# Optimization experiments

Measured on AMD Instinct MI355X. Metric: run time of the kernel, lower is better.

Reference implementation:

```python
import jax, jax.numpy as jnp
import numpy as np

SCALE = 15.0
BIG = 1e9  # masked-out distances; exp(-SCALE*BIG) underflows to exactly 0 in fp32
P, M, N, D, NCAM = 6, 512, 4096, 1024, 8
FEAT_STD = 0.03  # keep squared distances O(1) so exp(-scale*d) doesn't underflow


def setup_inputs() -> dict:
    key = jax.random.key(0)
    k1, k2, k3, k4 = jax.random.split(key, 4)
    feature = jax.random.normal(k1, (P, M, D), dtype=jnp.float32) * FEAT_STD
    centers = jax.random.normal(k2, (P, N, D), dtype=jnp.float32) * FEAT_STD
    camid = jax.random.randint(k3, (M,), 0, NCAM)   # camera id per sample
    cam = jax.random.randint(k4, (N,), 0, NCAM)     # camera id per center
    return {"feature": feature, "camid": camid, "centers": centers, "cam": cam}


def _explog(x):
    # faithful to torch: (-scale * x).exp().sum().log(), per row (last axis)
    return jnp.log(jnp.sum(jnp.exp(-SCALE * x), axis=-1))


def reference(feature, camid, centers, cam):
    p, m, d = feature.shape
    n = centers.shape[1]
    # squared euclidean distance map per part: [P, m, n]
    f2 = jnp.sum(feature * feature, axis=-1)            # [P, m]
    c2 = jnp.sum(centers * centers, axis=-1)            # [P, n]
    dist = f2[:, :, None] + c2[:, None, :] - 2.0 * jnp.einsum('pmd,pnd->pmn', feature, centers)
    # intra mask: center cam == sample cam  (same for all parts)
    mask = camid[:, None] == cam[None, :]               # [m, n]
    # push masked-out entries to BIG so ascending sort puts them last and exp(-s*BIG)=0
    d_intra = jnp.sort(jnp.where(mask[None, :, :], dist, BIG), axis=-1)   # [P, m, n]
    d_inter = jnp.sort(jnp.where(mask[None, :, :], BIG, dist), axis=-1)   # [P, m, n]
    x_intra = _explog(d_intra[..., :4])
    y_intra = _explog(d_intra[..., 6:])
    x_inter = _explog(d_inter[..., :8])
    y_inter = _explog(d_inter[..., 12:])
    hinge_intra = jnp.maximum(-x_intra + y_intra + 12.0, 0.0)
    hinge_inter = jnp.maximum(-x_inter + y_inter + 5.0, 0.0)
    loss = jnp.sum(hinge_intra + hinge_inter) / (m * p)
    return loss
```

## Files before the change

### kernel.cpp

```cpp
#include <hip/hip_runtime.h>
#include <math.h>

#define PP 6
#define MM 512
#define NN 4096
#define DD 1024
#define KSCALE 15.0f
#define BIGV 1e9f

#define BM 128
#define BN 128
#define BK 32
#define NCHUNK (DD / BK)
#define NSTRIP (NN / BN)
#define KI 6
#define KR 12
#define PARTW 20

typedef __bf16 bf16x8 __attribute__((ext_vector_type(8)));
typedef float  f32x16 __attribute__((ext_vector_type(16)));

__device__ __forceinline__ void insert6(float (&a)[KI], float v) {
    if (v < a[KI - 1]) {
        float cur = v;
#pragma unroll
        for (int x = 0; x < KI; ++x) {
            float lo = fminf(a[x], cur);
            float hi = fmaxf(a[x], cur);
            a[x] = lo; cur = hi;
        }
    }
}
__device__ __forceinline__ void insert12(float (&a)[KR], float v) {
    if (v < a[KR - 1]) {
        float cur = v;
#pragma unroll
        for (int x = 0; x < KR; ++x) {
            float lo = fminf(a[x], cur);
            float hi = fmaxf(a[x], cur);
            a[x] = lo; cur = hi;
        }
    }
}

__device__ __forceinline__ void cvt8(const float4& v0, const float4& v1,
                                     bf16x8& hi, bf16x8& lo) {
    float f[8] = {v0.x, v0.y, v0.z, v0.w, v1.x, v1.y, v1.z, v1.w};
#pragma unroll
    for (int i = 0; i < 8; ++i) {
        __bf16 h = (__bf16)f[i];
        hi[i] = h;
        lo[i] = (__bf16)(f[i] - (float)h);
    }
}

__device__ __forceinline__ float sq8(const float4& a, const float4& b) {
    float s = a.x * a.x;
    s = fmaf(a.y, a.y, s); s = fmaf(a.z, a.z, s); s = fmaf(a.w, a.w, s);
    s = fmaf(b.x, b.x, s); s = fmaf(b.y, b.y, s);
    s = fmaf(b.z, b.z, s); s = fmaf(b.w, b.w, s);
    return s;
}

__global__ __launch_bounds__(256, 2)
void dist_topk_kernel(const float* __restrict__ feature,
                      const int*   __restrict__ camid,
                      const float* __restrict__ centers,
                      const int*   __restrict__ cam,
                      float*       __restrict__ partials,
                      float*       __restrict__ out) {
    const int ns = blockIdx.x;
    const int mt = blockIdx.y;
    const int p  = blockIdx.z;
    const int t  = threadIdx.x;
    const int lane = t & 63, wid = t >> 6;
    const int wr = wid >> 1, wc = wid & 1;
    const int l31 = lane & 31, lh = lane >> 5;

    __shared__ __align__(16) char smem[128 * 129 * 4];
    __shared__ float c2buf[128][4];
    __shared__ int   s_cam[128];

    if (blockIdx.x == 0 && blockIdx.y == 0 && blockIdx.z == 0 && t == 0)
        out[0] = 0.0f;
    if (t < BN) s_cam[t] = cam[ns * BN + t];
    const int my_cam = camid[mt * BM + (t & 127)];

    const int sk = t & 3;
    const int srow = t >> 2;
    const float* Abase = feature + ((size_t)p * MM + mt * BM) * DD;
    const float* Bbase = centers + ((size_t)p * NN + ns * BN) * DD;

    const int wA0 = (sk * 128 + (srow ^ sk)) * 16;
    const int wA1 = (sk * 128 + ((srow + 64) ^ sk)) * 16;

    int aoff[2][2], boff[2][2];
#pragma unroll
    for (int s = 0; s < 2; ++s) {
        int ks = 2 * s + lh;
#pragma unroll
        for (int q = 0; q < 2; ++q) {
            int row = wr * 64 + q * 32 + l31;
            int col = wc * 64 + q * 32 + l31;
            aoff[q][s] = (ks * 128 + (row ^ ks)) * 16;
            boff[q][s] = (ks * 128 + (col ^ ks)) * 16;
        }
    }

    f32x16 acc[2][2];
#pragma unroll
    for (int i = 0; i < 2; ++i)
#pragma unroll
        for (int j = 0; j < 2; ++j)
#pragma unroll
            for (int r = 0; r < 16; ++r) acc[i][j][r] = 0.0f;

    float c2p0 = 0.0f, c2p1 = 0.0f;

    const float4* gA0 = (const float4*)(Abase + (size_t)srow * DD) + sk * 2;
    const float4* gA1 = (const float4*)(Abase + (size_t)(srow + 64) * DD) + sk * 2;
    const float4* gB0 = (const float4*)(Bbase + (size_t)srow * DD) + sk * 2;
    const float4* gB1 = (const float4*)(Bbase + (size_t)(srow + 64) * DD) + sk * 2;

    auto stage_write = [&](int buf,
                           const float4& a00, const float4& a01,
                           const float4& a10, const float4& a11,
                           const float4& b00, const float4& b01,
                           const float4& b10, const float4& b11) {
        char* base = smem + buf * 32768;
        bf16x8 hi, lo;
        cvt8(a00, a01, hi, lo);
        *(bf16x8*)(base + 0     + wA0) = hi;
        *(bf16x8*)(base + 8192  + wA0) = lo;
        cvt8(a10, a11, hi, lo);
        *(bf16x8*)(base + 0     + wA1) = hi;
        *(bf16x8*)(base + 8192  + wA1) = lo;
        cvt8(b00, b01, hi, lo);
        *(bf16x8*)(base + 16384 + wA0) = hi;
        *(bf16x8*)(base + 24576 + wA0) = lo;
        cvt8(b10, b11, hi, lo);
        *(bf16x8*)(base + 16384 + wA1) = hi;
        *(bf16x8*)(base + 24576 + wA1) = lo;
        c2p0 += sq8(b00, b01);
        c2p1 += sq8(b10, b11);
    };

    {
        float4 a00 = gA0[0], a01 = gA0[1], a10 = gA1[0], a11 = gA1[1];
        float4 b00 = gB0[0], b01 = gB0[1], b10 = gB1[0], b11 = gB1[1];
        stage_write(0, a00, a01, a10, a11, b00, b01, b10, b11);
    }
    __syncthreads();

    for (int c = 0; c < NCHUNK; ++c) {
        const int cur = c & 1;
        float4 na00, na01, na10, na11, nb00, nb01, nb10, nb11;
        if (c + 1 < NCHUNK) {
            const int o = (c + 1) * 8;
            na00 = gA0[o]; na01 = gA0[o + 1];
            na10 = gA1[o]; na11 = gA1[o + 1];
            nb00 = gB0[o]; nb01 = gB0[o + 1];
            nb10 = gB1[o]; nb11 = gB1[o + 1];
        }
        const char* bb = smem + cur * 32768;
#pragma unroll
        for (int s = 0; s < 2; ++s) {
            bf16x8 ahi[2], alo[2], bhi[2], blo[2];
#pragma unroll
            for (int q = 0; q < 2; ++q) {
                ahi[q] = *(const bf16x8*)(bb + 0     + aoff[q][s]);
                alo[q] = *(const bf16x8*)(bb + 8192  + aoff[q][s]);
                bhi[q] = *(const bf16x8*)(bb + 16384 + boff[q][s]);
                blo[q] = *(const bf16x8*)(bb + 24576 + boff[q][s]);
            }
#pragma unroll
            for (int mi = 0; mi < 2; ++mi)
#pragma unroll
                for (int nj = 0; nj < 2; ++nj) {
                    acc[mi][nj] = __builtin_amdgcn_mfma_f32_32x32x16_bf16(
                        ahi[mi], bhi[nj], acc[mi][nj], 0, 0, 0);
                    acc[mi][nj] = __builtin_amdgcn_mfma_f32_32x32x16_bf16(
                        ahi[mi], blo[nj], acc[mi][nj], 0, 0, 0);
                    acc[mi][nj] = __builtin_amdgcn_mfma_f32_32x32x16_bf16(
                        alo[mi], bhi[nj], acc[mi][nj], 0, 0, 0);
                }
        }
        if (c + 1 < NCHUNK)
            stage_write(cur ^ 1, na00, na01, na10, na11, nb00, nb01, nb10, nb11);
        __syncthreads();
    }

    c2buf[srow][sk]      = c2p0;
    c2buf[srow + 64][sk] = c2p1;
    __syncthreads();

    float* distS = (float*)smem;
    float c2v[2];
#pragma unroll
    for (int nj = 0; nj < 2; ++nj) {
        int C = wc * 64 + nj * 32 + l31;
        float4 q = *(const float4*)&c2buf[C][0];
        c2v[nj] = (q.x + q.y) + (q.z + q.w);
    }
#pragma unroll
    for (int mi = 0; mi < 2; ++mi)
#pragma unroll
        for (int nj = 0; nj < 2; ++nj) {
            int C = wc * 64 + nj * 32 + l31;
#pragma unroll
            for (int r = 0; r < 16; ++r) {
                int R = wr * 64 + mi * 32 + (r & 3) + 8 * (r >> 2) + 4 * lh;
                distS[R * 129 + C] = c2v[nj] - 2.0f * acc[mi][nj][r];
            }
        }
    __syncthreads();

    const int prow = t & 127, half = t >> 7;
    float ti[KI], tr[KR];
#pragma unroll
    for (int x = 0; x < KI; ++x) ti[x] = BIGV;
#pragma unroll
    for (int x = 0; x < KR; ++x) tr[x] = BIGV;
    float si = 0.0f, sr = 0.0f;
    const float* drow = distS + prow * 129 + half * 64;
    const int*   crow = s_cam + half * 64;
    for (int jj = 0; jj < 64; ++jj) {
        float dd = drow[jj];
        float e  = __expf(-KSCALE * dd);
        if (crow[jj] == my_cam) { si += e; insert6(ti, dd); }
        else                    { sr += e; insert12(tr, dd); }
    }
    __syncthreads();

    float* msh = (float*)smem;
    {
        float* mine = msh + t * PARTW;
#pragma unroll
        for (int x = 0; x < KI; ++x) mine[x] = ti[x];
#pragma unroll
        for (int x = 0; x < KR; ++x) mine[KI + x] = tr[x];
        mine[18] = si; mine[19] = sr;
    }
    __syncthreads();
    if (t < 128) {
        const float* oth = msh + (t + 128) * PARTW;
#pragma unroll
        for (int x = 0; x < KI; ++x) insert6(ti, oth[x]);
#pragma unroll
        for (int x = 0; x < KR; ++x) insert12(tr, oth[KI + x]);
        si += oth[18]; sr += oth[19];
        float* outp = partials +
            ((size_t)(p * MM + mt * BM + t) * NSTRIP + ns) * PARTW;
#pragma unroll
        for (int x = 0; x < KI; ++x) outp[x] = ti[x];
#pragma unroll
        for (int x = 0; x < KR; ++x) outp[KI + x] = tr[x];
        outp[18] = si; outp[19] = sr;
    }
}

__global__ __launch_bounds__(256)
void finalize_kernel(const float* __restrict__ partials, float* __restrict__ out) {
    const int t   = threadIdx.x;
    const int row = blockIdx.x * 256 + t;
    float ti[KI], tr[KR];
#pragma unroll
    for (int x = 0; x < KI; ++x) ti[x] = BIGV;
#pragma unroll
    for (int x = 0; x < KR; ++x) tr[x] = BIGV;
    float si = 0.0f, sr = 0.0f;
    const float* base = partials + (size_t)row * NSTRIP * PARTW;
    for (int s = 0; s < NSTRIP; ++s) {
        const float* q = base + s * PARTW;
#pragma unroll
        for (int x = 0; x < KI; ++x) insert6(ti, q[x]);
#pragma unroll
        for (int x = 0; x < KR; ++x) insert12(tr, q[KI + x]);
        si += q[18]; sr += q[19];
    }
    float ei[KI], er[KR];
#pragma unroll
    for (int x = 0; x < KI; ++x) ei[x] = __expf(-KSCALE * ti[x]);
#pragma unroll
    for (int x = 0; x < KR; ++x) er[x] = __expf(-KSCALE * tr[x]);
    float x_intra = logf(ei[0] + ei[1] + ei[2] + ei[3]);
    float top6 = ei[0] + ei[1] + ei[2] + ei[3] + ei[4] + ei[5];
    float y_intra = logf(fmaxf(si - top6, 0.0f));
    float x_inter = logf(er[0] + er[1] + er[2] + er[3] +
                         er[4] + er[5] + er[6] + er[7]);
    float top12 = 0.0f;
#pragma unroll
    for (int x = 0; x < KR; ++x) top12 += er[x];
    float y_inter = logf(fmaxf(sr - top12, 0.0f));
    float h = fmaxf(y_intra - x_intra + 12.0f, 0.0f) +
              fmaxf(y_inter - x_inter + 5.0f, 0.0f);

    __shared__ float red[256];
    red[t] = h;
    __syncthreads();
#pragma unroll
    for (int s = 128; s > 0; s >>= 1) {
        if (t < s) red[t] += red[t + s];
        __syncthreads();
    }
    if (t == 0) atomicAdd(out, red[0] * (1.0f / (MM * PP)));
}

extern "C" void kernel_launch(void* const* d_in, const int* in_sizes, int n_in,
                              void* d_out, int out_size, void* d_ws, size_t ws_size,
                              hipStream_t stream) {
    const float* feature = (const float*)d_in[0];
    const int*   camid   = (const int*)  d_in[1];
    const float* centers = (const float*)d_in[2];
    const int*   cam     = (const int*)  d_in[3];
    float* out = (float*)d_out;

    float* partials = (float*)d_ws;

    dim3 grid(NSTRIP, MM / BM, PP);
    dist_topk_kernel<<<grid, 256, 0, stream>>>(feature, camid, centers, cam,
                                               partials, out);
    finalize_kernel<<<(PP * MM) / 256, 256, 0, stream>>>(partials, out);
}
```

Before: 412.0 us.

## Pre-split inputs into bf16 hi/lo planes and stream via global_load_lds

Adds two prep kernels that split feature and centers into bf16 hi/lo planes, with c2 norms computed once in the centers kernel. The main kernel then stages tiles into LDS with direct global-to-LDS loads at BK=16 instead of converting in registers, and targets 3 blocks per CU. The epilogue writes distances through a small 32-column band buffer and merges the two half-rows with wave shuffles. Finalize now reduces across strips with shuffles, one row per wave. The cost is an extra pass that writes and rereads about 113MB of bf16 workspace, more barriers per K step, and smaller K chunks.

```diff
diff --git a/kernel.cpp b/kernel.cpp
--- a/kernel.cpp
+++ b/kernel.cpp
@@ -10,12 +10,13 @@
 
 #define BM 128
 #define BN 128
-#define BK 32
+#define BK 16
 #define NCHUNK (DD / BK)
 #define NSTRIP (NN / BN)
 #define KI 6
 #define KR 12
 #define PARTW 20
+#define LDSB 16384
 
 typedef __bf16 bf16x8 __attribute__((ext_vector_type(8)));
 typedef float  f32x16 __attribute__((ext_vector_type(16)));
@@ -43,68 +44,97 @@
     }
 }
 
-__device__ __forceinline__ void cvt8(const float4& v0, const float4& v1,
-                                     bf16x8& hi, bf16x8& lo) {
-    float f[8] = {v0.x, v0.y, v0.z, v0.w, v1.x, v1.y, v1.z, v1.w};
+
+__global__ __launch_bounds__(256)
+void decomp_feat(const float* __restrict__ f,
+                 __bf16* __restrict__ hi, __bf16* __restrict__ lo) {
+    size_t base = ((size_t)blockIdx.x * 256 + threadIdx.x) * 8;
+    float4 v0 = *(const float4*)(f + base);
+    float4 v1 = *(const float4*)(f + base + 4);
+    float fv[8] = {v0.x, v0.y, v0.z, v0.w, v1.x, v1.y, v1.z, v1.w};
+    bf16x8 h, l;
 #pragma unroll
     for (int i = 0; i < 8; ++i) {
-        __bf16 h = (__bf16)f[i];
-        hi[i] = h;
-        lo[i] = (__bf16)(f[i] - (float)h);
-    }
-}
-
-__device__ __forceinline__ float sq8(const float4& a, const float4& b) {
-    float s = a.x * a.x;
-    s = fmaf(a.y, a.y, s); s = fmaf(a.z, a.z, s); s = fmaf(a.w, a.w, s);
-    s = fmaf(b.x, b.x, s); s = fmaf(b.y, b.y, s);
-    s = fmaf(b.z, b.z, s); s = fmaf(b.w, b.w, s);
-    return s;
-}
-
-__global__ __launch_bounds__(256, 2)
-void dist_topk_kernel(const float* __restrict__ feature,
-                      const int*   __restrict__ camid,
-                      const float* __restrict__ centers,
-                      const int*   __restrict__ cam,
-                      float*       __restrict__ partials,
-                      float*       __restrict__ out) {
+        __bf16 hh = (__bf16)fv[i];
+        h[i] = hh;
+        l[i] = (__bf16)(fv[i] - (float)hh);
+    }
+    *(bf16x8*)(hi + base) = h;
+    *(bf16x8*)(lo + base) = l;
+}
+
+__global__ __launch_bounds__(256)
+void decomp_cent(const float* __restrict__ cz,
+                 __bf16* __restrict__ hi, __bf16* __restrict__ lo,
+                 float* __restrict__ c2, float* __restrict__ out) {
+    if (blockIdx.x == 0 && threadIdx.x == 0) out[0] = 0.0f;
+    const int row  = blockIdx.x * 4 + (threadIdx.x >> 6);
+    const int lane = threadIdx.x & 63;
+    const size_t eb = (size_t)row * DD + lane * 16;
+    float s = 0.0f;
+#pragma unroll
+    for (int g = 0; g < 2; ++g) {
+        float4 v0 = *(const float4*)(cz + eb + g * 8);
+        float4 v1 = *(const float4*)(cz + eb + g * 8 + 4);
+        float fv[8] = {v0.x, v0.y, v0.z, v0.w, v1.x, v1.y, v1.z, v1.w};
+        bf16x8 h, l;
+#pragma unroll
+        for (int i = 0; i < 8; ++i) {
+            s = fmaf(fv[i], fv[i], s);
+            __bf16 hh = (__bf16)fv[i];
+            h[i] = hh;
+            l[i] = (__bf16)(fv[i] - (float)hh);
+        }
+        *(bf16x8*)(hi + eb + g * 8) = h;
+        *(bf16x8*)(lo + eb + g * 8) = l;
+    }
+#pragma unroll
+    for (int off = 32; off > 0; off >>= 1) s += __shfl_down(s, off, 64);
+    if (lane == 0) c2[row] = s;
+}
+
+
+__global__ __launch_bounds__(256, 3)
+void dist_topk_kernel(const __bf16* __restrict__ Fhi, const __bf16* __restrict__ Flo,
+                      const __bf16* __restrict__ Chi, const __bf16* __restrict__ Clo,
+                      const float* __restrict__ c2g,
+                      const int* __restrict__ camid, const int* __restrict__ cam,
+                      float* __restrict__ partials) {
     const int ns = blockIdx.x;
     const int mt = blockIdx.y;
     const int p  = blockIdx.z;
     const int t  = threadIdx.x;
-    const int lane = t & 63, wid = t >> 6;
-    const int wr = wid >> 1, wc = wid & 1;
+    const int lane = t & 63, w = t >> 6;
+    const int wr = w >> 1, wc = w & 1;
     const int l31 = lane & 31, lh = lane >> 5;
 
-    __shared__ __align__(16) char smem[128 * 129 * 4];
-    __shared__ float c2buf[128][4];
-    __shared__ int   s_cam[128];
-
-    if (blockIdx.x == 0 && blockIdx.y == 0 && blockIdx.z == 0 && t == 0)
-        out[0] = 0.0f;
+    __shared__ __align__(16) char smem[2 * LDSB + 128 * 33 * 4];
+    __shared__ int s_cam[BN];
+    float* bandS = (float*)(smem + 2 * LDSB);
+
     if (t < BN) s_cam[t] = cam[ns * BN + t];
-    const int my_cam = camid[mt * BM + (t & 127)];
-
-    const int sk = t & 3;
-    const int srow = t >> 2;
-    const float* Abase = feature + ((size_t)p * MM + mt * BM) * DD;
-    const float* Bbase = centers + ((size_t)p * NN + ns * BN) * DD;
-
-    const int wA0 = (sk * 128 + (srow ^ sk)) * 16;
-    const int wA1 = (sk * 128 + ((srow + 64) ^ sk)) * 16;
-
-    int aoff[2][2], boff[2][2];
-#pragma unroll
-    for (int s = 0; s < 2; ++s) {
-        int ks = 2 * s + lh;
-#pragma unroll
-        for (int q = 0; q < 2; ++q) {
-            int row = wr * 64 + q * 32 + l31;
-            int col = wc * 64 + q * 32 + l31;
-            aoff[q][s] = (ks * 128 + (row ^ ks)) * 16;
-            boff[q][s] = (ks * 128 + (col ^ ks)) * 16;
-        }
+
+    const char* srcp[4];
+    int ldsoff[4];
+#pragma unroll
+    for (int i = 0; i < 4; ++i) {
+        const int r_idx = w * 4 + i;
+        const int plane = r_idx >> 3;
+        const int ks    = (r_idx >> 2) & 1;
+        const int row   = (r_idx & 3) * 64 + lane;
+        const __bf16* basep;
+        size_t gr;
+        if (row < BM) { basep = plane ? Flo : Fhi; gr = (size_t)(p * MM + mt * BM + row) * DD; }
+        else          { basep = plane ? Clo : Chi; gr = (size_t)(p * NN + ns * BN + row - BM) * DD; }
+        srcp[i]   = (const char*)(basep + gr + ks * 8);
+        ldsoff[i] = r_idx * 1024;
+    }
+
+    int aU[2], bU[2];
+#pragma unroll
+    for (int x = 0; x < 2; ++x) {
+        aU[x] = (lh * 256 + wr * 64 + x * 32 + l31) * 16;
+        bU[x] = (lh * 256 + 128 + wc * 64 + x * 32 + l31) * 16;
     }
 
     f32x16 acc[2][2];
@@ -115,142 +145,98 @@
 #pragma unroll
             for (int r = 0; r < 16; ++r) acc[i][j][r] = 0.0f;
 
-    float c2p0 = 0.0f, c2p1 = 0.0f;
-
-    const float4* gA0 = (const float4*)(Abase + (size_t)srow * DD) + sk * 2;
-    const float4* gA1 = (const float4*)(Abase + (size_t)(srow + 64) * DD) + sk * 2;
-    const float4* gB0 = (const float4*)(Bbase + (size_t)srow * DD) + sk * 2;
-    const float4* gB1 = (const float4*)(Bbase + (size_t)(srow + 64) * DD) + sk * 2;
-
-    auto stage_write = [&](int buf,
-                           const float4& a00, const float4& a01,
-                           const float4& a10, const float4& a11,
-                           const float4& b00, const float4& b01,
-                           const float4& b10, const float4& b11) {
-        char* base = smem + buf * 32768;
-        bf16x8 hi, lo;
-        cvt8(a00, a01, hi, lo);
-        *(bf16x8*)(base + 0     + wA0) = hi;
-        *(bf16x8*)(base + 8192  + wA0) = lo;
-        cvt8(a10, a11, hi, lo);
-        *(bf16x8*)(base + 0     + wA1) = hi;
-        *(bf16x8*)(base + 8192  + wA1) = lo;
-        cvt8(b00, b01, hi, lo);
-        *(bf16x8*)(base + 16384 + wA0) = hi;
-        *(bf16x8*)(base + 24576 + wA0) = lo;
-        cvt8(b10, b11, hi, lo);
-        *(bf16x8*)(base + 16384 + wA1) = hi;
-        *(bf16x8*)(base + 24576 + wA1) = lo;
-        c2p0 += sq8(b00, b01);
-        c2p1 += sq8(b10, b11);
+    auto stage = [&](int buf, int c) {
+#pragma unroll
+        for (int i = 0; i < 4; ++i)
+            __builtin_amdgcn_global_load_lds(
+                (const __attribute__((address_space(1))) void*)(srcp[i] + (size_t)c * 32),
+                (__attribute__((address_space(3))) void*)(smem + buf * LDSB + ldsoff[i]),
+                16, 0, 0);
     };
 
-    {
-        float4 a00 = gA0[0], a01 = gA0[1], a10 = gA1[0], a11 = gA1[1];
-        float4 b00 = gB0[0], b01 = gB0[1], b10 = gB1[0], b11 = gB1[1];
-        stage_write(0, a00, a01, a10, a11, b00, b01, b10, b11);
-    }
+    stage(0, 0);
     __syncthreads();
 
     for (int c = 0; c < NCHUNK; ++c) {
         const int cur = c & 1;
-        float4 na00, na01, na10, na11, nb00, nb01, nb10, nb11;
-        if (c + 1 < NCHUNK) {
-            const int o = (c + 1) * 8;
-            na00 = gA0[o]; na01 = gA0[o + 1];
-            na10 = gA1[o]; na11 = gA1[o + 1];
-            nb00 = gB0[o]; nb01 = gB0[o + 1];
-            nb10 = gB1[o]; nb11 = gB1[o + 1];
-        }
-        const char* bb = smem + cur * 32768;
-#pragma unroll
-        for (int s = 0; s < 2; ++s) {
-            bf16x8 ahi[2], alo[2], bhi[2], blo[2];
-#pragma unroll
-            for (int q = 0; q < 2; ++q) {
-                ahi[q] = *(const bf16x8*)(bb + 0     + aoff[q][s]);
-                alo[q] = *(const bf16x8*)(bb + 8192  + aoff[q][s]);
-                bhi[q] = *(const bf16x8*)(bb + 16384 + boff[q][s]);
-                blo[q] = *(const bf16x8*)(bb + 24576 + boff[q][s]);
+        if (c + 1 < NCHUNK) stage(cur ^ 1, c + 1);
+        const char* bb = smem + cur * LDSB;
+        bf16x8 ah[2], al[2], bh[2], bl[2];
+#pragma unroll
+        for (int x = 0; x < 2; ++x) {
+            ah[x] = *(const bf16x8*)(bb + aU[x]);
+            al[x] = *(const bf16x8*)(bb + 8192 + aU[x]);
+            bh[x] = *(const bf16x8*)(bb + bU[x]);
+            bl[x] = *(const bf16x8*)(bb + 8192 + bU[x]);
+        }
+#pragma unroll
+        for (int mi = 0; mi < 2; ++mi)
+#pragma unroll
+            for (int nj = 0; nj < 2; ++nj) {
+                acc[mi][nj] = __builtin_amdgcn_mfma_f32_32x32x16_bf16(
+                    ah[mi], bh[nj], acc[mi][nj], 0, 0, 0);
+                acc[mi][nj] = __builtin_amdgcn_mfma_f32_32x32x16_bf16(
+                    ah[mi], bl[nj], acc[mi][nj], 0, 0, 0);
+                acc[mi][nj] = __builtin_amdgcn_mfma_f32_32x32x16_bf16(
+                    al[mi], bh[nj], acc[mi][nj], 0, 0, 0);
             }
-#pragma unroll
-            for (int mi = 0; mi < 2; ++mi)
-#pragma unroll
-                for (int nj = 0; nj < 2; ++nj) {
-                    acc[mi][nj] = __builtin_amdgcn_mfma_f32_32x32x16_bf16(
-                        ahi[mi], bhi[nj], acc[mi][nj], 0, 0, 0);
-                    acc[mi][nj] = __builtin_amdgcn_mfma_f32_32x32x16_bf16(
-                        ahi[mi], blo[nj], acc[mi][nj], 0, 0, 0);
-                    acc[mi][nj] = __builtin_amdgcn_mfma_f32_32x32x16_bf16(
-                        alo[mi], bhi[nj], acc[mi][nj], 0, 0, 0);
-                }
-        }
-        if (c + 1 < NCHUNK)
-            stage_write(cur ^ 1, na00, na01, na10, na11, nb00, nb01, nb10, nb11);
         __syncthreads();
     }
 
-    c2buf[srow][sk]      = c2p0;
-    c2buf[srow + 64][sk] = c2p1;
-    __syncthreads();
-
-    float* distS = (float*)smem;
     float c2v[2];
 #pragma unroll
-    for (int nj = 0; nj < 2; ++nj) {
-        int C = wc * 64 + nj * 32 + l31;
-        float4 q = *(const float4*)&c2buf[C][0];
-        c2v[nj] = (q.x + q.y) + (q.z + q.w);
-    }
-#pragma unroll
-    for (int mi = 0; mi < 2; ++mi)
-#pragma unroll
-        for (int nj = 0; nj < 2; ++nj) {
-            int C = wc * 64 + nj * 32 + l31;
-#pragma unroll
-            for (int r = 0; r < 16; ++r) {
-                int R = wr * 64 + mi * 32 + (r & 3) + 8 * (r >> 2) + 4 * lh;
-                distS[R * 129 + C] = c2v[nj] - 2.0f * acc[mi][nj][r];
-            }
-        }
-    __syncthreads();
-
-    const int prow = t & 127, half = t >> 7;
+    for (int nj = 0; nj < 2; ++nj)
+        c2v[nj] = c2g[p * NN + ns * BN + wc * 64 + nj * 32 + l31];
+
+    const int myrow = t >> 1, half = t & 1;
+    const int my_cam = camid[mt * BM + myrow];
     float ti[KI], tr[KR];
 #pragma unroll
     for (int x = 0; x < KI; ++x) ti[x] = BIGV;
 #pragma unroll
     for (int x = 0; x < KR; ++x) tr[x] = BIGV;
     float si = 0.0f, sr = 0.0f;
-    const float* drow = distS + prow * 129 + half * 64;
-    const int*   crow = s_cam + half * 64;
-    for (int jj = 0; jj < 64; ++jj) {
-        float dd = drow[jj];
-        float e  = __expf(-KSCALE * dd);
-        if (crow[jj] == my_cam) { si += e; insert6(ti, dd); }
-        else                    { sr += e; insert12(tr, dd); }
-    }
-    __syncthreads();
-
-    float* msh = (float*)smem;
-    {
-        float* mine = msh + t * PARTW;
-#pragma unroll
-        for (int x = 0; x < KI; ++x) mine[x] = ti[x];
-#pragma unroll
-        for (int x = 0; x < KR; ++x) mine[KI + x] = tr[x];
-        mine[18] = si; mine[19] = sr;
-    }
-    __syncthreads();
-    if (t < 128) {
-        const float* oth = msh + (t + 128) * PARTW;
-#pragma unroll
-        for (int x = 0; x < KI; ++x) insert6(ti, oth[x]);
-#pragma unroll
-        for (int x = 0; x < KR; ++x) insert12(tr, oth[KI + x]);
-        si += oth[18]; sr += oth[19];
+
+#pragma unroll
+    for (int b = 0; b < 4; ++b) {
+        __syncthreads();
+        if (wc == (b >> 1)) {
+            const int nj = b & 1;
+#pragma unroll
+            for (int mi = 0; mi < 2; ++mi)
+#pragma unroll
+                for (int r = 0; r < 16; ++r) {
+                    int R = wr * 64 + mi * 32 + (r & 3) + 8 * (r >> 2) + 4 * lh;
+                    bandS[R * 33 + l31] = c2v[nj] - 2.0f * acc[mi][nj][r];
+                }
+        }
+        __syncthreads();
+        const float* drow = bandS + myrow * 33 + half * 16;
+        const int*   crow = s_cam + b * 32 + half * 16;
+#pragma unroll
+        for (int j = 0; j < 16; ++j) {
+            float dd = drow[j];
+            float e  = __expf(-KSCALE * dd);
+            if (crow[j] == my_cam) { si += e; insert6(ti, dd); }
+            else                   { sr += e; insert12(tr, dd); }
+        }
+    }
+
+    float oti[KI], otr[KR];
+#pragma unroll
+    for (int x = 0; x < KI; ++x) oti[x] = __shfl_xor(ti[x], 1, 64);
+#pragma unroll
+    for (int x = 0; x < KR; ++x) otr[x] = __shfl_xor(tr[x], 1, 64);
+    float osi = __shfl_xor(si, 1, 64), osr = __shfl_xor(sr, 1, 64);
+#pragma unroll
+    for (int x = 0; x < KI; ++x) insert6(ti, oti[x]);
+#pragma unroll
+    for (int x = 0; x < KR; ++x) insert12(tr, otr[x]);
+    si += osi; sr += osr;
+
+    if (!half) {
         float* outp = partials +
-            ((size_t)(p * MM + mt * BM + t) * NSTRIP + ns) * PARTW;
+            ((size_t)(p * MM + mt * BM + myrow) * NSTRIP + ns) * PARTW;
 #pragma unroll
         for (int x = 0; x < KI; ++x) outp[x] = ti[x];
 #pragma unroll
@@ -259,51 +245,54 @@
     }
 }
 
+
 __global__ __launch_bounds__(256)
 void finalize_kernel(const float* __restrict__ partials, float* __restrict__ out) {
-    const int t   = threadIdx.x;
-    const int row = blockIdx.x * 256 + t;
+    const int t = threadIdx.x, lane = t & 63, w = t >> 6;
+    const int row = blockIdx.x * 4 + w;
+    const int strip = lane & 31;
+    const float* q = partials + ((size_t)row * NSTRIP + strip) * PARTW;
     float ti[KI], tr[KR];
 #pragma unroll
-    for (int x = 0; x < KI; ++x) ti[x] = BIGV;
-#pragma unroll
-    for (int x = 0; x < KR; ++x) tr[x] = BIGV;
-    float si = 0.0f, sr = 0.0f;
-    const float* base = partials + (size_t)row * NSTRIP * PARTW;
-    for (int s = 0; s < NSTRIP; ++s) {
-        const float* q = base + s * PARTW;
-#pragma unroll
-        for (int x = 0; x < KI; ++x) insert6(ti, q[x]);
-#pragma unroll
-        for (int x = 0; x < KR; ++x) insert12(tr, q[KI + x]);
-        si += q[18]; sr += q[19];
-    }
-    float ei[KI], er[KR];
-#pragma unroll
-    for (int x = 0; x < KI; ++x) ei[x] = __expf(-KSCALE * ti[x]);
-#pragma unroll
-    for (int x = 0; x < KR; ++x) er[x] = __expf(-KSCALE * tr[x]);
-    float x_intra = logf(ei[0] + ei[1] + ei[2] + ei[3]);
-    float top6 = ei[0] + ei[1] + ei[2] + ei[3] + ei[4] + ei[5];
-    float y_intra = logf(fmaxf(si - top6, 0.0f));
-    float x_inter = logf(er[0] + er[1] + er[2] + er[3] +
-                         er[4] + er[5] + er[6] + er[7]);
-    float top12 = 0.0f;
-#pragma unroll
-    for (int x = 0; x < KR; ++x) top12 += er[x];
-    float y_inter = logf(fmaxf(sr - top12, 0.0f));
-    float h = fmaxf(y_intra - x_intra + 12.0f, 0.0f) +
-              fmaxf(y_inter - x_inter + 5.0f, 0.0f);
-
-    __shared__ float red[256];
-    red[t] = h;
-    __syncthreads();
-#pragma unroll
-    for (int s = 128; s > 0; s >>= 1) {
-        if (t < s) red[t] += red[t + s];
-        __syncthreads();
-    }
-    if (t == 0) atomicAdd(out, red[0] * (1.0f / (MM * PP)));
+    for (int x = 0; x < KI; ++x) ti[x] = q[x];
+#pragma unroll
+    for (int x = 0; x < KR; ++x) tr[x] = q[KI + x];
+    float si = q[18], sr = q[19];
+
+#pragma unroll
+    for (int s = 1; s < 32; s <<= 1) {
+        float oti[KI], otr[KR];
+#pragma unroll
+        for (int x = 0; x < KI; ++x) oti[x] = __shfl_xor(ti[x], s, 64);
+#pragma unroll
+        for (int x = 0; x < KR; ++x) otr[x] = __shfl_xor(tr[x], s, 64);
+        float osi = __shfl_xor(si, s, 64), osr = __shfl_xor(sr, s, 64);
+#pragma unroll
+        for (int x = 0; x < KI; ++x) insert6(ti, oti[x]);
+#pragma unroll
+        for (int x = 0; x < KR; ++x) insert12(tr, otr[x]);
+        si += osi; sr += osr;
+    }
+
+    if (lane == 0) {
+        float ei[KI], er[KR];
+#pragma unroll
+        for (int x = 0; x < KI; ++x) ei[x] = __expf(-KSCALE * ti[x]);
+#pragma unroll
+        for (int x = 0; x < KR; ++x) er[x] = __expf(-KSCALE * tr[x]);
+        float x_intra = logf(ei[0] + ei[1] + ei[2] + ei[3]);
+        float top6 = ei[0] + ei[1] + ei[2] + ei[3] + ei[4] + ei[5];
+        float y_intra = logf(fmaxf(si - top6, 0.0f));
+        float x_inter = logf(er[0] + er[1] + er[2] + er[3] +
+                             er[4] + er[5] + er[6] + er[7]);
+        float top12 = 0.0f;
+#pragma unroll
+        for (int x = 0; x < KR; ++x) top12 += er[x];
+        float y_inter = logf(fmaxf(sr - top12, 0.0f));
+        float h = fmaxf(y_intra - x_intra + 12.0f, 0.0f) +
+                  fmaxf(y_inter - x_inter + 5.0f, 0.0f);
+        atomicAdd(out, h * (1.0f / (MM * PP)));
+    }
 }
 
 extern "C" void kernel_launch(void* const* d_in, const int* in_sizes, int n_in,
@@ -315,10 +304,18 @@
     const int*   cam     = (const int*)  d_in[3];
     float* out = (float*)d_out;
 
-    float* partials = (float*)d_ws;
-
+    char* ws = (char*)d_ws;
+    __bf16* Chi = (__bf16*)(ws);
+    __bf16* Clo = (__bf16*)(ws + 50331648);
+    __bf16* Fhi = (__bf16*)(ws + 100663296);
+    __bf16* Flo = (__bf16*)(ws + 106954752);
+    float*  c2  = (float*) (ws + 113246208);
+    float*  partials = (float*)(ws + 113344512);
+
+    decomp_feat<<<(PP * MM * DD / 8) / 256, 256, 0, stream>>>(feature, Fhi, Flo);
+    decomp_cent<<<(PP * NN) / 4, 256, 0, stream>>>(centers, Chi, Clo, c2, out);
     dim3 grid(NSTRIP, MM / BM, PP);
-    dist_topk_kernel<<<grid, 256, 0, stream>>>(feature, camid, centers, cam,
-                                               partials, out);
-    finalize_kernel<<<(PP * MM) / 256, 256, 0, stream>>>(partials, out);
-}
+    dist_topk_kernel<<<grid, 256, 0, stream>>>(Fhi, Flo, Chi, Clo, c2,
+                                               camid, cam, partials);
+    finalize_kernel<<<(PP * MM) / 4, 256, 0, stream>>>(partials, out);
+}
```

Measured after the change: 358.3 us. -13.0%, faster.
